# Kernel optimization log

Measured on AMD Instinct MI355X. Metric: run time of the kernel, lower is better.

## Reference

```python
import jax, jax.numpy as jnp
import numpy as np

N = 50000      # nodes
E = 800000     # edges
C = 128        # dim_feat / channels
D = 256        # dim_dense
OUT = 2        # dim_out
L = 5          # num_layers - 1 GCN2Conv layers
ALPHA = 0.1    # main_param -> GCN2Conv alpha; theta=None -> beta=1.0
SLOPE = 0.01   # LeakyReLU default negative slope


def setup_inputs() -> dict:
    key = jax.random.key(0)
    ks = jax.random.split(key, 6)
    x = jax.random.normal(ks[0], (N, C), jnp.float32)
    edge_index = jax.random.randint(ks[1], (2, E), 0, N, jnp.int32)
    conv_weights = jax.random.normal(ks[2], (L, C, C), jnp.float32) * (1.0 / np.sqrt(C))
    w_dense = jax.random.normal(ks[3], (C, D), jnp.float32) * (1.0 / np.sqrt(C))
    b_dense = jnp.zeros((D,), jnp.float32)
    w_out = jax.random.normal(ks[4], (D, OUT), jnp.float32) * (1.0 / np.sqrt(D))
    b_out = jnp.zeros((OUT,), jnp.float32)
    return dict(x=x, edge_index=edge_index, conv_weights=conv_weights,
                w_dense=w_dense, b_dense=b_dense, w_out=w_out, b_out=b_out)


def _gcn_norm(edge_index, num_nodes):
    """Symmetric gcn_norm with self-loops: returns row, col, D^-1/2 * D^-1/2 edge weights."""
    loop = jnp.arange(num_nodes, dtype=edge_index.dtype)
    row = jnp.concatenate([edge_index[0], loop])  # sources
    col = jnp.concatenate([edge_index[1], loop])  # targets (aggregation index)
    ones = jnp.ones(row.shape[0], jnp.float32)
    deg = jax.ops.segment_sum(ones, col, num_segments=num_nodes)
    dinv = jnp.where(deg > 0, jax.lax.rsqrt(jnp.maximum(deg, 1e-12)), 0.0)
    return row, col, dinv[row] * dinv[col]


def reference(x, edge_index, conv_weights, w_dense, b_dense, w_out, b_out):
    num_nodes = x.shape[0]
    row, col, norm = _gcn_norm(edge_index, num_nodes)
    x0 = x
    for l in range(conv_weights.shape[0]):
        # propagate: h[i] = sum_{j->i} norm * x[j]   (gather -> scatter-add)
        h = jax.ops.segment_sum(norm[:, None] * x[row], col, num_segments=num_nodes)
        # GCN2Conv with shared_weights=True, beta=1 (theta=None): out = ((1-a)h + a*x0) @ W
        out = (1.0 - ALPHA) * h + ALPHA * x0
        x = jax.nn.leaky_relu(out @ conv_weights[l], negative_slope=SLOPE)
    x = x @ w_dense + b_dense
    return x @ w_out + b_out
```

## Files before the change

### kernel.cpp

```cpp
#include <hip/hip_runtime.h>
#include <hip/hip_fp16.h>

#define C 128
#define NOUT 2
#define ALPHA 0.1f
#define SLOPE 0.01f
#define ZP 136

typedef _Float16 half4v __attribute__((ext_vector_type(4)));
typedef float float4v __attribute__((ext_vector_type(4)));


__global__ __launch_bounds__(256) void count_prep_kernel(
    const int* __restrict__ col, int* __restrict__ cnt8, int* __restrict__ rank, int E,
    const float* __restrict__ x, __half* __restrict__ xh, int n,
    const float* __restrict__ W, _Float16* __restrict__ WT, int wtot,
    const float* __restrict__ wd, _Float16* __restrict__ WDT,
    int CB, int CV, int WTB)
{
    int b = blockIdx.x;
    if (b < CB) {
        int* mycnt = cnt8 + (size_t)(b & 7) * n;
        int base = b * 2048 + threadIdx.x;
        #pragma unroll
        for (int j = 0; j < 8; ++j) {
            int e = base + j * 256;
            if (e < E) rank[e] = atomicAdd(&mycnt[col[e]], 1);
        }
    } else if (b < CB + CV) {
        int g = (b - CB) * 256 + threadIdx.x;
        if (g >= n * 32) return;
        float4 v = ((const float4*)x)[g];
        union { __half2 h; unsigned u; } a2, b2;
        a2.h = __float22half2_rn(make_float2(v.x, v.y));
        b2.h = __float22half2_rn(make_float2(v.z, v.w));
        ((uint2*)xh)[g] = make_uint2(a2.u, b2.u);
    } else if (b < CB + CV + WTB) {
        int idx = (b - CB - CV) * 256 + threadIdx.x;
        if (idx >= wtot) return;
        int l = idx >> 14, rem = idx & 16383;
        int nrow = rem >> 7, kk = rem & 127;
        WT[idx] = (_Float16)W[(l << 14) + kk * C + nrow];
    } else {
        int idx = (b - CB - CV - WTB) * 256 + threadIdx.x;
        if (idx >= 256 * C) return;
        int nrow = idx >> 7, kk = idx & 127;
        WDT[idx] = (_Float16)wd[kk * 256 + nrow];
    }
}

__global__ __launch_bounds__(1024) void scanA_kernel(int* __restrict__ cnt8,
                                                     int* __restrict__ offs,
                                                     int* __restrict__ bsum,
                                                     float* __restrict__ dinv, int n) {
    __shared__ int wsum[16];
    int t = threadIdx.x, lane = t & 63, wv = t >> 6;
    int i = blockIdx.x * 1024 + t;
    int v = 0;
    if (i < n) {
        int s = 0;
        #pragma unroll
        for (int j = 0; j < 8; ++j) {
            size_t idx = (size_t)j * n + i;
            int cj = cnt8[idx];
            cnt8[idx] = s;
            s += cj;
        }
        v = s;
        dinv[i] = rsqrtf((float)(v + 1));
    }
    int sc = v;
    #pragma unroll
    for (int d = 1; d < 64; d <<= 1) {
        int u = __shfl_up(sc, d);
        if (lane >= d) sc += u;
    }
    if (lane == 63) wsum[wv] = sc;
    __syncthreads();
    int woff = 0;
    #pragma unroll
    for (int j = 0; j < 16; ++j) woff += (j < wv) ? wsum[j] : 0;
    if (i < n) offs[i] = woff + sc - v;
    if (t == 0) {
        int tot = 0;
        #pragma unroll
        for (int j = 0; j < 16; ++j) tot += wsum[j];
        bsum[blockIdx.x] = tot;
    }
}

__global__ __launch_bounds__(1024) void scanB_kernel(const int* __restrict__ bsum,
                                                     int* __restrict__ bbase, int nb) {
    __shared__ int wsum[16];
    int t = threadIdx.x, lane = t & 63, wv = t >> 6;
    int v = (t < nb) ? bsum[t] : 0;
    int sc = v;
    #pragma unroll
    for (int d = 1; d < 64; d <<= 1) {
        int u = __shfl_up(sc, d);
        if (lane >= d) sc += u;
    }
    if (lane == 63) wsum[wv] = sc;
    __syncthreads();
    int woff = 0;
    #pragma unroll
    for (int j = 0; j < 16; ++j) woff += (j < wv) ? wsum[j] : 0;
    if (t < nb) bbase[t] = woff + sc - v;
}

__global__ void scanC_kernel(int* __restrict__ offs, const int* __restrict__ bbase,
                             int n, int E) {
    int i = blockIdx.x * 256 + threadIdx.x;
    if (i < n) offs[i] = offs[i] + bbase[i >> 10];
    if (i == n) offs[n] = E;
}

__global__ void fill_kernel(const int* __restrict__ row, const int* __restrict__ col,
                            const float* __restrict__ dinv, const int* __restrict__ offs,
                            const int* __restrict__ rank, const int* __restrict__ cnt8,
                            unsigned* __restrict__ csr, int E, int n) {
    int base = blockIdx.x * 2048 + threadIdx.x;
    #pragma unroll
    for (int j = 0; j < 8; ++j) {
        int e = base + j * 256;
        if (e < E) {
            int r = row[e], c = col[e];
            int copy = (e >> 11) & 7;
            int rk = rank[e] + cnt8[(size_t)copy * n + c];
            union { __half h; unsigned short u; } nh;
            nh.h = __float2half_rn(dinv[r] * dinv[c]);
            csr[offs[c] + rk] = ((unsigned)r << 16) | (unsigned)nh.u;
        }
    }
}

__device__ __forceinline__ void accum8(float* a, uint4 q, float w) {
    union { unsigned u; __half2 h; } c;
    float2 f;
    c.u = q.x; f = __half22float2(c.h); a[0] += w * f.x; a[1] += w * f.y;
    c.u = q.y; f = __half22float2(c.h); a[2] += w * f.x; a[3] += w * f.y;
    c.u = q.z; f = __half22float2(c.h); a[4] += w * f.x; a[5] += w * f.y;
    c.u = q.w; f = __half22float2(c.h); a[6] += w * f.x; a[7] += w * f.y;
}

__device__ __forceinline__ uint4 pack8(const float* a) {
    union { __half2 h; unsigned u; } c0, c1, c2, c3;
    c0.h = __float22half2_rn(make_float2(a[0], a[1]));
    c1.h = __float22half2_rn(make_float2(a[2], a[3]));
    c2.h = __float22half2_rn(make_float2(a[4], a[5]));
    c3.h = __float22half2_rn(make_float2(a[6], a[7]));
    return make_uint4(c0.u, c1.u, c2.u, c3.u);
}

__device__ __forceinline__ float norm_of(unsigned m) {
    union { unsigned short u; __half h; } nh;
    nh.u = (unsigned short)(m & 0xffffu);
    return __half2float(nh.h);
}

__global__ __launch_bounds__(256) void agg_kernel(
    const __half* __restrict__ xc, const __half* __restrict__ x0h,
    const int* __restrict__ offs, const unsigned* __restrict__ csr,
    const float* __restrict__ dinv, __half* __restrict__ z, int n)
{
    int node = blockIdx.x * 8 + (threadIdx.x >> 5);
    if (node >= n) return;
    int l32 = threadIdx.x & 31;
    int sub = l32 >> 4;
    int cg = l32 & 15;
    const uint4* x4 = (const uint4*)xc;
    uint4 qs = x4[(size_t)node * 16 + cg];
    uint4 q0x = ((const uint4*)x0h)[(size_t)node * 16 + cg];
    float di = dinv[node];

    float a0[8] = {}, a1[8] = {}, a2[8] = {}, a3[8] = {};
    int beg = offs[node], end = offs[node + 1];
    int k = beg + sub;
    for (; k + 14 < end; k += 16) {
        unsigned m0 = csr[k], m1 = csr[k + 2], m2 = csr[k + 4], m3 = csr[k + 6];
        unsigned m4 = csr[k + 8], m5 = csr[k + 10], m6 = csr[k + 12], m7 = csr[k + 14];
        uint4 q0 = x4[(size_t)(m0 >> 16) * 16 + cg];
        uint4 q1 = x4[(size_t)(m1 >> 16) * 16 + cg];
        uint4 q2 = x4[(size_t)(m2 >> 16) * 16 + cg];
        uint4 q3 = x4[(size_t)(m3 >> 16) * 16 + cg];
        uint4 q4 = x4[(size_t)(m4 >> 16) * 16 + cg];
        uint4 q5 = x4[(size_t)(m5 >> 16) * 16 + cg];
        uint4 q6 = x4[(size_t)(m6 >> 16) * 16 + cg];
        uint4 q7 = x4[(size_t)(m7 >> 16) * 16 + cg];
        accum8(a0, q0, norm_of(m0));
        accum8(a1, q1, norm_of(m1));
        accum8(a2, q2, norm_of(m2));
        accum8(a3, q3, norm_of(m3));
        accum8(a0, q4, norm_of(m4));
        accum8(a1, q5, norm_of(m5));
        accum8(a2, q6, norm_of(m6));
        accum8(a3, q7, norm_of(m7));
    }
    for (; k + 6 < end; k += 8) {
        unsigned m0 = csr[k], m1 = csr[k + 2], m2 = csr[k + 4], m3 = csr[k + 6];
        uint4 q0 = x4[(size_t)(m0 >> 16) * 16 + cg];
        uint4 q1 = x4[(size_t)(m1 >> 16) * 16 + cg];
        uint4 q2 = x4[(size_t)(m2 >> 16) * 16 + cg];
        uint4 q3 = x4[(size_t)(m3 >> 16) * 16 + cg];
        accum8(a0, q0, norm_of(m0));
        accum8(a1, q1, norm_of(m1));
        accum8(a2, q2, norm_of(m2));
        accum8(a3, q3, norm_of(m3));
    }
    for (; k < end; k += 2) {
        unsigned m = csr[k];
        uint4 q = x4[(size_t)(m >> 16) * 16 + cg];
        accum8(a0, q, norm_of(m));
    }
    #pragma unroll
    for (int j = 0; j < 8; ++j) a0[j] += a1[j] + a2[j] + a3[j];
    #pragma unroll
    for (int j = 0; j < 8; ++j) a0[j] += __shfl_xor(a0[j], 16);
    if (sub == 0) {
        float sw = di * di;
        accum8(a0, qs, sw);
        float xr[8] = {};
        accum8(xr, q0x, 1.f);
        float zz[8];
        #pragma unroll
        for (int j = 0; j < 8; ++j) zz[j] = (1.f - ALPHA) * a0[j] + ALPHA * xr[j];
        ((uint4*)z)[(size_t)node * 16 + cg] = pack8(zz);
    }
}

__global__ __launch_bounds__(256) void layer_mfma(
    const __half* __restrict__ zin, const _Float16* __restrict__ WT,
    __half* __restrict__ xn, int n)
{
    __shared__ _Float16 zl[64 * ZP];
    int i0 = blockIdx.x * 64;
    int t = threadIdx.x;
    int w = t >> 6, lane = t & 63;
    int c = lane & 15, g = lane >> 4;

    const uint4* z4 = (const uint4*)zin;
    #pragma unroll
    for (int p = t; p < 64 * 16; p += 256) {
        int r = p >> 4, c8 = p & 15;
        uint4 zv = make_uint4(0, 0, 0, 0);
        if (i0 + r < n) zv = z4[(size_t)(i0 + r) * 16 + c8];
        *(uint4*)&zl[r * ZP + c8 * 8] = zv;
    }

    half4v bf[8][2];
    #pragma unroll
    for (int kb = 0; kb < 8; ++kb)
        #pragma unroll
        for (int nt = 0; nt < 2; ++nt)
            bf[kb][nt] = *(const half4v*)&WT[((w * 2 + nt) * 16 + c) * C + kb * 16 + 4 * g];

    __syncthreads();

    #pragma unroll
    for (int m = 0; m < 4; ++m) {
        const _Float16* arow = &zl[(m * 16 + c) * ZP];
        half4v af[8];
        #pragma unroll
        for (int kb = 0; kb < 8; ++kb) af[kb] = *(const half4v*)&arow[kb * 16 + 4 * g];
        float4v acc0 = (float4v)0.f, acc1 = (float4v)0.f;
        #pragma unroll
        for (int kb = 0; kb < 8; ++kb) {
            acc0 = __builtin_amdgcn_mfma_f32_16x16x16f16(af[kb], bf[kb][0], acc0, 0, 0, 0);
            acc1 = __builtin_amdgcn_mfma_f32_16x16x16f16(af[kb], bf[kb][1], acc1, 0, 0, 0);
        }
        #pragma unroll
        for (int r = 0; r < 4; ++r) {
            int node = i0 + m * 16 + 4 * g + r;
            if (node < n) {
                float v0 = acc0[r]; v0 = v0 > 0.f ? v0 : SLOPE * v0;
                float v1 = acc1[r]; v1 = v1 > 0.f ? v1 : SLOPE * v1;
                xn[(size_t)node * C + w * 32 + c]      = __float2half_rn(v0);
                xn[(size_t)node * C + w * 32 + 16 + c] = __float2half_rn(v1);
            }
        }
    }
}

__global__ __launch_bounds__(256) void dense_mfma(
    const __half* __restrict__ xin, const _Float16* __restrict__ WDT,
    const float* __restrict__ bd, const float* __restrict__ wo,
    const float* __restrict__ bo, float* __restrict__ out, int n)
{
    __shared__ _Float16 xl[64 * ZP];
    __shared__ float pp[64][4][2];
    int i0 = blockIdx.x * 64;
    int t = threadIdx.x;
    int w = t >> 6, lane = t & 63;
    int c = lane & 15, g = lane >> 4;

    const uint4* g4 = (const uint4*)xin;
    for (int p = t; p < 64 * 16; p += 256) {
        int r = p >> 4, c8 = p & 15;
        uint4 v = make_uint4(0, 0, 0, 0);
        if (i0 + r < n) v = g4[(size_t)(i0 + r) * 16 + c8];
        *(uint4*)&xl[r * ZP + c8 * 8] = v;
    }

    half4v bf[8][4];
    #pragma unroll
    for (int kb = 0; kb < 8; ++kb)
        #pragma unroll
        for (int nt = 0; nt < 4; ++nt)
            bf[kb][nt] = *(const half4v*)&WDT[((w * 4 + nt) * 16 + c) * C + kb * 16 + 4 * g];
    float bdv[4], wo0[4], wo1[4];
    #pragma unroll
    for (int nt = 0; nt < 4; ++nt) {
        int coln = (w * 4 + nt) * 16 + c;
        bdv[nt] = bd[coln];
        wo0[nt] = wo[coln * 2 + 0];
        wo1[nt] = wo[coln * 2 + 1];
    }

    __syncthreads();

    #pragma unroll
    for (int m = 0; m < 4; ++m) {
        const _Float16* arow = &xl[(m * 16 + c) * ZP];
        half4v af[8];
        #pragma unroll
        for (int kb = 0; kb < 8; ++kb) af[kb] = *(const half4v*)&arow[kb * 16 + 4 * g];
        float4v acc[4];
        #pragma unroll
        for (int nt = 0; nt < 4; ++nt) acc[nt] = (float4v)0.f;
        #pragma unroll
        for (int kb = 0; kb < 8; ++kb) {
            #pragma unroll
            for (int nt = 0; nt < 4; ++nt)
                acc[nt] = __builtin_amdgcn_mfma_f32_16x16x16f16(af[kb], bf[kb][nt], acc[nt], 0, 0, 0);
        }
        float p0[4] = {0.f, 0.f, 0.f, 0.f}, p1[4] = {0.f, 0.f, 0.f, 0.f};
        #pragma unroll
        for (int nt = 0; nt < 4; ++nt) {
            #pragma unroll
            for (int r = 0; r < 4; ++r) {
                float hv = acc[nt][r] + bdv[nt];
                p0[r] += hv * wo0[nt];
                p1[r] += hv * wo1[nt];
            }
        }
        #pragma unroll
        for (int ms = 1; ms <= 8; ms <<= 1) {
            #pragma unroll
            for (int r = 0; r < 4; ++r) {
                p0[r] += __shfl_xor(p0[r], ms);
                p1[r] += __shfl_xor(p1[r], ms);
            }
        }
        if (c == 0) {
            #pragma unroll
            for (int r = 0; r < 4; ++r) {
                pp[m * 16 + 4 * g + r][w][0] = p0[r];
                pp[m * 16 + 4 * g + r][w][1] = p1[r];
            }
        }
    }
    __syncthreads();
    if (t < 128) {
        int r = t >> 1, o = t & 1;
        int node = i0 + r;
        if (node < n) {
            float s = pp[r][0][o] + pp[r][1][o] + pp[r][2][o] + pp[r][3][o];
            out[(size_t)node * NOUT + o] = s + bo[o];
        }
    }
}

extern "C" void kernel_launch(void* const* d_in, const int* in_sizes, int n_in,
                              void* d_out, int out_size, void* d_ws, size_t ws_size,
                              hipStream_t stream) {
    const float* x0    = (const float*)d_in[0];
    const int*   ei    = (const int*)d_in[1];
    const float* convW = (const float*)d_in[2];
    const float* wd    = (const float*)d_in[3];
    const float* bd    = (const float*)d_in[4];
    const float* wo    = (const float*)d_in[5];
    const float* bo    = (const float*)d_in[6];
    float* out = (float*)d_out;

    int N = in_sizes[0] / C;
    int E = in_sizes[1] / 2;
    int L = in_sizes[2] / (C * C);
    const int* row = ei;
    const int* col = ei + E;
    int NB = (N + 1023) / 1024;

    char* p = (char*)d_ws;
    auto alloc = [&](size_t bytes) {
        char* r = p;
        p += (bytes + 255) & ~(size_t)255;
        return r;
    };
    int*      cnt8   = (int*)alloc((size_t)8 * N * 4);
    int*      offs   = (int*)alloc((size_t)(N + 1) * 4);
    int*      rank   = (int*)alloc((size_t)E * 4);
    int*      bsum   = (int*)alloc((size_t)NB * 4);
    int*      bbase  = (int*)alloc((size_t)NB * 4);
    unsigned* csr    = (unsigned*)alloc((size_t)E * 4);
    float*    dinv   = (float*)alloc((size_t)N * 4);
    __half*   x0h    = (__half*)alloc((size_t)N * C * 2);
    __half*   bufA   = (__half*)alloc((size_t)N * C * 2);
    __half*   zbuf   = (__half*)alloc((size_t)N * C * 2);
    _Float16* WT     = (_Float16*)alloc((size_t)L * C * C * 2);
    _Float16* WDT    = (_Float16*)alloc((size_t)256 * C * 2);

    int wtot = L * C * C;
    int CB  = (E + 2047) / 2048;
    int CV  = (N * 32 + 255) / 256;
    int WTB = (wtot + 255) / 256;
    int WDB = (256 * C + 255) / 256;

    hipMemsetAsync(cnt8, 0, (size_t)8 * N * 4, stream);
    count_prep_kernel<<<CB + CV + WTB + WDB, 256, 0, stream>>>(
        col, cnt8, rank, E, x0, x0h, N, convW, WT, wtot, wd, WDT, CB, CV, WTB);
    scanA_kernel<<<NB, 1024, 0, stream>>>(cnt8, offs, bsum, dinv, N);
    scanB_kernel<<<1, 1024, 0, stream>>>(bsum, bbase, NB);
    scanC_kernel<<<(N + 256) / 256, 256, 0, stream>>>(offs, bbase, N, E);
    fill_kernel<<<(E + 2047) / 2048, 256, 0, stream>>>(row, col, dinv, offs, rank,
                                                       cnt8, csr, E, N);

    const __half* xc = x0h;
    for (int l = 0; l < L; ++l) {
        agg_kernel<<<(N + 7) / 8, 256, 0, stream>>>(xc, x0h, offs, csr, dinv, zbuf, N);
        layer_mfma<<<(N + 63) / 64, 256, 0, stream>>>(zbuf, WT + (size_t)l * C * C,
                                                      bufA, N);
        xc = bufA;
    }
    dense_mfma<<<(N + 63) / 64, 256, 0, stream>>>(xc, WDT, bd, wo, bo, out, N);
}
```

Measured before the change: 368.7 us.

## Split node features into four channel chunks so gathers hit smaller working sets

Feature buffers are re-laid out as four channel-major chunks of 32 halves per node, covering x0h, z and the layer outputs. The aggregation kernel now processes one chunk per block, with 4 lanes per node instead of 32. Each gather pass therefore touches a quarter-size array that fits better in L2/MALL. The CSR index loads become nontemporal, and the MFMA kernels reassemble chunks when staging into LDS. The cost is that each edge index is now read four times, one gather is split into 64-byte pieces, and the MFMA output stores become strided per chunk.

```diff
diff --git a/kernel.cpp b/kernel.cpp
--- a/kernel.cpp
+++ b/kernel.cpp
@@ -6,6 +6,7 @@
 #define ALPHA 0.1f
 #define SLOPE 0.01f
 #define ZP 136
+#define NCH 4
 
 typedef _Float16 half4v __attribute__((ext_vector_type(4)));
 typedef float float4v __attribute__((ext_vector_type(4)));
@@ -30,11 +31,14 @@
     } else if (b < CB + CV) {
         int g = (b - CB) * 256 + threadIdx.x;
         if (g >= n * 32) return;
+        int node = g >> 5, c4q = g & 31;
         float4 v = ((const float4*)x)[g];
         union { __half2 h; unsigned u; } a2, b2;
         a2.h = __float22half2_rn(make_float2(v.x, v.y));
         b2.h = __float22half2_rn(make_float2(v.z, v.w));
-        ((uint2*)xh)[g] = make_uint2(a2.u, b2.u);
+        int chunk = c4q >> 3, pos = c4q & 7;
+        ((uint2*)xh)[(size_t)chunk * (n * 8) + (size_t)node * 8 + pos] =
+            make_uint2(a2.u, b2.u);
     } else if (b < CB + CV + WTB) {
         int idx = (b - CB - CV) * 256 + threadIdx.x;
         if (idx >= wtot) return;
@@ -163,30 +167,35 @@
     const int* __restrict__ offs, const unsigned* __restrict__ csr,
     const float* __restrict__ dinv, __half* __restrict__ z, int n)
 {
-    int node = blockIdx.x * 8 + (threadIdx.x >> 5);
+    int chunk = blockIdx.x & 3;
+    int node = (blockIdx.x >> 2) * 64 + (threadIdx.x >> 2);
     if (node >= n) return;
-    int l32 = threadIdx.x & 31;
-    int sub = l32 >> 4;
-    int cg = l32 & 15;
-    const uint4* x4 = (const uint4*)xc;
-    uint4 qs = x4[(size_t)node * 16 + cg];
-    uint4 q0x = ((const uint4*)x0h)[(size_t)node * 16 + cg];
+    int ln = threadIdx.x & 3;
+    const uint4* x4 = (const uint4*)xc + (size_t)chunk * n * 4;
+    const uint4* x04 = (const uint4*)x0h + (size_t)chunk * n * 4;
+    uint4 qs = x4[(size_t)node * 4 + ln];
+    uint4 q0x = x04[(size_t)node * 4 + ln];
     float di = dinv[node];
 
     float a0[8] = {}, a1[8] = {}, a2[8] = {}, a3[8] = {};
-    int beg = offs[node], end = offs[node + 1];
-    int k = beg + sub;
-    for (; k + 14 < end; k += 16) {
-        unsigned m0 = csr[k], m1 = csr[k + 2], m2 = csr[k + 4], m3 = csr[k + 6];
-        unsigned m4 = csr[k + 8], m5 = csr[k + 10], m6 = csr[k + 12], m7 = csr[k + 14];
-        uint4 q0 = x4[(size_t)(m0 >> 16) * 16 + cg];
-        uint4 q1 = x4[(size_t)(m1 >> 16) * 16 + cg];
-        uint4 q2 = x4[(size_t)(m2 >> 16) * 16 + cg];
-        uint4 q3 = x4[(size_t)(m3 >> 16) * 16 + cg];
-        uint4 q4 = x4[(size_t)(m4 >> 16) * 16 + cg];
-        uint4 q5 = x4[(size_t)(m5 >> 16) * 16 + cg];
-        uint4 q6 = x4[(size_t)(m6 >> 16) * 16 + cg];
-        uint4 q7 = x4[(size_t)(m7 >> 16) * 16 + cg];
+    int k = offs[node], end = offs[node + 1];
+    for (; k + 7 < end; k += 8) {
+        unsigned m0 = __builtin_nontemporal_load(&csr[k + 0]);
+        unsigned m1 = __builtin_nontemporal_load(&csr[k + 1]);
+        unsigned m2 = __builtin_nontemporal_load(&csr[k + 2]);
+        unsigned m3 = __builtin_nontemporal_load(&csr[k + 3]);
+        unsigned m4 = __builtin_nontemporal_load(&csr[k + 4]);
+        unsigned m5 = __builtin_nontemporal_load(&csr[k + 5]);
+        unsigned m6 = __builtin_nontemporal_load(&csr[k + 6]);
+        unsigned m7 = __builtin_nontemporal_load(&csr[k + 7]);
+        uint4 q0 = x4[(size_t)(m0 >> 16) * 4 + ln];
+        uint4 q1 = x4[(size_t)(m1 >> 16) * 4 + ln];
+        uint4 q2 = x4[(size_t)(m2 >> 16) * 4 + ln];
+        uint4 q3 = x4[(size_t)(m3 >> 16) * 4 + ln];
+        uint4 q4 = x4[(size_t)(m4 >> 16) * 4 + ln];
+        uint4 q5 = x4[(size_t)(m5 >> 16) * 4 + ln];
+        uint4 q6 = x4[(size_t)(m6 >> 16) * 4 + ln];
+        uint4 q7 = x4[(size_t)(m7 >> 16) * 4 + ln];
         accum8(a0, q0, norm_of(m0));
         accum8(a1, q1, norm_of(m1));
         accum8(a2, q2, norm_of(m2));
@@ -196,36 +205,28 @@
         accum8(a2, q6, norm_of(m6));
         accum8(a3, q7, norm_of(m7));
     }
-    for (; k + 6 < end; k += 8) {
-        unsigned m0 = csr[k], m1 = csr[k + 2], m2 = csr[k + 4], m3 = csr[k + 6];
-        uint4 q0 = x4[(size_t)(m0 >> 16) * 16 + cg];
-        uint4 q1 = x4[(size_t)(m1 >> 16) * 16 + cg];
-        uint4 q2 = x4[(size_t)(m2 >> 16) * 16 + cg];
-        uint4 q3 = x4[(size_t)(m3 >> 16) * 16 + cg];
+    for (; k + 1 < end; k += 2) {
+        unsigned m0 = __builtin_nontemporal_load(&csr[k + 0]);
+        unsigned m1 = __builtin_nontemporal_load(&csr[k + 1]);
+        uint4 q0 = x4[(size_t)(m0 >> 16) * 4 + ln];
+        uint4 q1 = x4[(size_t)(m1 >> 16) * 4 + ln];
         accum8(a0, q0, norm_of(m0));
         accum8(a1, q1, norm_of(m1));
-        accum8(a2, q2, norm_of(m2));
-        accum8(a3, q3, norm_of(m3));
-    }
-    for (; k < end; k += 2) {
-        unsigned m = csr[k];
-        uint4 q = x4[(size_t)(m >> 16) * 16 + cg];
+    }
+    if (k < end) {
+        unsigned m = __builtin_nontemporal_load(&csr[k]);
+        uint4 q = x4[(size_t)(m >> 16) * 4 + ln];
         accum8(a0, q, norm_of(m));
     }
-    #pragma unroll
-    for (int j = 0; j < 8; ++j) a0[j] += a1[j] + a2[j] + a3[j];
-    #pragma unroll
-    for (int j = 0; j < 8; ++j) a0[j] += __shfl_xor(a0[j], 16);
-    if (sub == 0) {
-        float sw = di * di;
-        accum8(a0, qs, sw);
-        float xr[8] = {};
-        accum8(xr, q0x, 1.f);
-        float zz[8];
-        #pragma unroll
-        for (int j = 0; j < 8; ++j) zz[j] = (1.f - ALPHA) * a0[j] + ALPHA * xr[j];
-        ((uint4*)z)[(size_t)node * 16 + cg] = pack8(zz);
-    }
+    float sw = di * di;
+    accum8(a0, qs, sw);
+    float xr[8] = {};
+    accum8(xr, q0x, 1.f);
+    float zz[8];
+    #pragma unroll
+    for (int j = 0; j < 8; ++j)
+        zz[j] = (1.f - ALPHA) * (a0[j] + a1[j] + a2[j] + a3[j]) + ALPHA * xr[j];
+    ((uint4*)z)[(size_t)chunk * n * 4 + (size_t)node * 4 + ln] = pack8(zz);
 }
 
 __global__ __launch_bounds__(256) void layer_mfma(
@@ -240,11 +241,14 @@
 
     const uint4* z4 = (const uint4*)zin;
     #pragma unroll
-    for (int p = t; p < 64 * 16; p += 256) {
-        int r = p >> 4, c8 = p & 15;
+    for (int q = 0; q < 4; ++q) {
+        int idx = q * 256 + t;
+        int chunk = idx >> 8;
+        int within = idx & 255;
+        int r = within >> 2, u = within & 3;
         uint4 zv = make_uint4(0, 0, 0, 0);
-        if (i0 + r < n) zv = z4[(size_t)(i0 + r) * 16 + c8];
-        *(uint4*)&zl[r * ZP + c8 * 8] = zv;
+        if (i0 + r < n) zv = z4[(size_t)chunk * n * 4 + (size_t)(i0 + r) * 4 + u];
+        *(uint4*)&zl[r * ZP + chunk * 32 + u * 8] = zv;
     }
 
     half4v bf[8][2];
@@ -274,8 +278,8 @@
             if (node < n) {
                 float v0 = acc0[r]; v0 = v0 > 0.f ? v0 : SLOPE * v0;
                 float v1 = acc1[r]; v1 = v1 > 0.f ? v1 : SLOPE * v1;
-                xn[(size_t)node * C + w * 32 + c]      = __float2half_rn(v0);
-                xn[(size_t)node * C + w * 32 + 16 + c] = __float2half_rn(v1);
+                xn[(size_t)w * (n * 32) + (size_t)node * 32 + c]      = __float2half_rn(v0);
+                xn[(size_t)w * (n * 32) + (size_t)node * 32 + 16 + c] = __float2half_rn(v1);
             }
         }
     }
@@ -294,11 +298,15 @@
     int c = lane & 15, g = lane >> 4;
 
     const uint4* g4 = (const uint4*)xin;
-    for (int p = t; p < 64 * 16; p += 256) {
-        int r = p >> 4, c8 = p & 15;
+    #pragma unroll
+    for (int q = 0; q < 4; ++q) {
+        int idx = q * 256 + t;
+        int chunk = idx >> 8;
+        int within = idx & 255;
+        int r = within >> 2, u = within & 3;
         uint4 v = make_uint4(0, 0, 0, 0);
-        if (i0 + r < n) v = g4[(size_t)(i0 + r) * 16 + c8];
-        *(uint4*)&xl[r * ZP + c8 * 8] = v;
+        if (i0 + r < n) v = g4[(size_t)chunk * n * 4 + (size_t)(i0 + r) * 4 + u];
+        *(uint4*)&xl[r * ZP + chunk * 32 + u * 8] = v;
     }
 
     half4v bf[8][4];
@@ -414,7 +422,7 @@
     int WTB = (wtot + 255) / 256;
     int WDB = (256 * C + 255) / 256;
 
-    hipMemsetAsync(cnt8, 0, (size_t)8 * N * 4, stream);
+    (void)hipMemsetAsync(cnt8, 0, (size_t)8 * N * 4, stream);
     count_prep_kernel<<<CB + CV + WTB + WDB, 256, 0, stream>>>(
         col, cnt8, rank, E, x0, x0h, N, convW, WT, wtot, wd, WDT, CB, CV, WTB);
     scanA_kernel<<<NB, 1024, 0, stream>>>(cnt8, offs, bsum, dinv, N);
@@ -424,8 +432,9 @@
                                                        cnt8, csr, E, N);
 
     const __half* xc = x0h;
+    int aggGrid = ((N + 63) / 64) * NCH;
     for (int l = 0; l < L; ++l) {
-        agg_kernel<<<(N + 7) / 8, 256, 0, stream>>>(xc, x0h, offs, csr, dinv, zbuf, N);
+        agg_kernel<<<aggGrid, 256, 0, stream>>>(xc, x0h, offs, csr, dinv, zbuf, N);
         layer_mfma<<<(N + 63) / 64, 256, 0, stream>>>(zbuf, WT + (size_t)l * C * C,
                                                       bufA, N);
         xc = bufA;
```

Result: slower. 411.7 us (+11.7%).
